# Kernel optimization log

Hardware: AMD Instinct MI355X
Metric: run time of the kernel (lower is better)

## Reference

```python
import jax, jax.numpy as jnp
import numpy as np

EPS = 1e-7
MAX_TAN_NORM = 10.0  # safe_expmap0 clamp


def logmap0(x):
    # x: [..., D] Lorentz point, x[..., 0] = time component (>= 1)
    x0 = x[..., :1]
    xs = x[..., 1:]
    d = jnp.arccosh(jnp.clip(x0, 1.0 + EPS, None))          # geodesic distance to origin
    ns = jnp.clip(jnp.linalg.norm(xs, axis=-1, keepdims=True), EPS, None)
    return jnp.concatenate([jnp.zeros_like(x0), d * xs / ns], axis=-1)


def safe_expmap0(u):
    # u: tangent at origin; time component is projected out (proju at origin)
    us = u[..., 1:]
    n = jnp.clip(jnp.linalg.norm(us, axis=-1, keepdims=True), EPS, None)
    nc = jnp.minimum(n, MAX_TAN_NORM)                        # clamp norm for stability
    usc = us * (nc / n)
    return jnp.concatenate([jnp.cosh(nc), jnp.sinh(nc) * usc / nc], axis=-1)


def projx(x):
    # re-project onto the hyperboloid: x0 = sqrt(1 + ||xs||^2)
    xs = x[..., 1:]
    x0 = jnp.sqrt(1.0 + jnp.sum(xs * xs, axis=-1, keepdims=True))
    return jnp.concatenate([x0, xs], axis=-1)


def lorentz_linear(x_hyp, W, b):
    t = logmap0(x_hyp)
    y = t @ W.T + b
    return projx(safe_expmap0(y))


def setup_inputs() -> dict:
    key = jax.random.key(0)
    ks = jax.random.split(key, 8)
    N, D_IN, D_HID, D_OUT = 8192, 1024, 4096, 1024
    s = 0.02
    x_sp = jax.random.normal(ks[0], (N, D_IN), dtype=jnp.float32)
    x_hyp = projx(x_sp)  # valid Lorentz point (time comp overwritten)
    W1 = jax.random.normal(ks[1], (D_HID, D_IN), dtype=jnp.float32) * s
    b1 = jnp.zeros((D_HID,), dtype=jnp.float32)
    W2 = jax.random.normal(ks[2], (D_HID, D_HID), dtype=jnp.float32) * s
    b2 = jnp.zeros((D_HID,), dtype=jnp.float32)
    W3 = jax.random.normal(ks[3], (D_OUT, D_HID), dtype=jnp.float32) * s
    b3 = jnp.zeros((D_OUT,), dtype=jnp.float32)
    return {"x_hyp": x_hyp, "W1": W1, "b1": b1, "W2": W2, "b2": b2, "W3": W3, "b3": b3}


def reference(x_hyp, W1, b1, W2, b2, W3, b3):
    # layers[:-1] with inter-layer logmap0 -> (dropout=identity in eval) -> expmap0 -> projx
    h = lorentz_linear(x_hyp, W1, b1)
    h = projx(safe_expmap0(logmap0(h)))
    h = lorentz_linear(h, W2, b2)
    h = projx(safe_expmap0(logmap0(h)))
    return lorentz_linear(h, W3, b3)
```

## Files before the change

### kernel.cpp

```cpp
#include <hip/hip_runtime.h>
#include <stdint.h>

#define EPSF 1e-7f
#define MAXTAN 10.0f

typedef __bf16 bf16x8 __attribute__((ext_vector_type(8)));
typedef float floatx4 __attribute__((ext_vector_type(4)));
typedef __attribute__((address_space(3))) void lds_void_t;
typedef __attribute__((address_space(1))) void gbl_void_t;

__device__ __forceinline__ unsigned short f2bf(float x) {
  union { float f; uint32_t u; } v; v.f = x;
  uint32_t u = v.u;
  u += 0x7fffu + ((u >> 16) & 1u);
  return (unsigned short)(u >> 16);
}
__device__ __forceinline__ float bf2f(unsigned short h) {
  union { uint32_t u; float f; } v; v.u = ((uint32_t)h) << 16;
  return v.f;
}

__device__ __forceinline__ int sniff_mode(const unsigned short* x) {
  int sane = 0;
  for (int i = 0; i < 128; ++i) {
    unsigned short h = x[i];
    int e = (h >> 7) & 0xFF;
    if ((h & 0x7FFF) == 0 || (e >= 96 && e <= 140)) ++sane;
  }
  return (sane >= 120) ? 1 : 0;
}

__global__ void k_init(const unsigned short* __restrict__ x, int* __restrict__ modeg,
                       const void* __restrict__ b1, const void* __restrict__ b2,
                       const void* __restrict__ b3, float* __restrict__ o1,
                       float* __restrict__ o2, float* __restrict__ o3) {
  __shared__ int mds;
  if (threadIdx.x == 0) {
    int m = sniff_mode(x);
    mds = m;
    if (blockIdx.x == 0) *modeg = m;
  }
  __syncthreads();
  int m = mds;
  int i = blockIdx.x * 256 + threadIdx.x;
  if (i < 4096) o1[i] = m ? bf2f(((const unsigned short*)b1)[i]) : ((const float*)b1)[i];
  if (i < 4096) o2[i] = m ? bf2f(((const unsigned short*)b2)[i]) : ((const float*)b2)[i];
  if (i < 1024) o3[i] = m ? bf2f(((const unsigned short*)b3)[i]) : ((const float*)b3)[i];
}

__global__ void k_prep(const void* __restrict__ xv, unsigned short* __restrict__ xb,
                       float* __restrict__ sc0, float* __restrict__ x0c,
                       const int* __restrict__ mode) {
  const int row = blockIdx.x;
  const int tid = threadIdx.x;
  float4 v;
  if (*mode) {
    ushort4 u = ((const ushort4*)((const unsigned short*)xv + (size_t)row * 1024))[tid];
    v.x = bf2f(u.x); v.y = bf2f(u.y); v.z = bf2f(u.z); v.w = bf2f(u.w);
  } else {
    v = ((const float4*)((const float*)xv + (size_t)row * 1024))[tid];
  }
  ushort4 o;
  o.x = f2bf(v.x); o.y = f2bf(v.y); o.z = f2bf(v.z); o.w = f2bf(v.w);
  ((ushort4*)(xb + (size_t)row * 1024))[tid] = o;

  float s = v.x * v.x + v.y * v.y + v.z * v.z + v.w * v.w;
  if (tid == 0) s -= v.x * v.x;
  for (int off = 32; off; off >>= 1) s += __shfl_down(s, off, 64);
  __shared__ float red[4];
  if ((tid & 63) == 0) red[tid >> 6] = s;
  __syncthreads();
  if (tid == 0) {
    s = red[0] + red[1] + red[2] + red[3];
    float ns = fmaxf(sqrtf(s), EPSF);
    float d = acoshf(fmaxf(v.x, 1.0f + EPSF));
    sc0[row] = d / ns;
    x0c[row] = bf2f(o.x);
  }
}

template<int K8>
__global__ void k_cvtw(const void* __restrict__ in, unsigned short* __restrict__ out,
                       const int* __restrict__ mode, int n8, float* __restrict__ c0) {
  int i = blockIdx.x * 256 + threadIdx.x;
  if (i >= n8) return;
  if (*mode) {
    uint4 g = ((const uint4*)in)[i];
    ((uint4*)out)[i] = g;
    if (i % K8 == 0) c0[i / K8] = bf2f((unsigned short)(g.x & 0xFFFFu));
  } else {
    float4 a = ((const float4*)in)[2 * i];
    float4 b = ((const float4*)in)[2 * i + 1];
    ushort4 oa, ob;
    oa.x = f2bf(a.x); oa.y = f2bf(a.y); oa.z = f2bf(a.z); oa.w = f2bf(a.w);
    ob.x = f2bf(b.x); ob.y = f2bf(b.y); ob.z = f2bf(b.z); ob.w = f2bf(b.w);
    ((ushort4*)out)[2 * i] = oa;
    ((ushort4*)out)[2 * i + 1] = ob;
    if (i % K8 == 0) c0[i / K8] = bf2f(oa.x);
  }
}

template<int NBLK>
__global__ void k_sc(const float* __restrict__ part, const unsigned short* __restrict__ y,
                     int stride, float* __restrict__ sc, float* __restrict__ c0,
                     float* __restrict__ ssout, int nrows) {
  int i = blockIdx.x * 256 + threadIdx.x;
  if (i >= nrows) return;
  float s = 0.f;
#pragma unroll
  for (int j = 0; j < NBLK; ++j) s += part[(size_t)i * NBLK + j];
  float n = fmaxf(sqrtf(fmaxf(s, 0.f)), EPSF);
  sc[i] = fminf(n, MAXTAN) / n;
  c0[i] = bf2f(y[(size_t)i * stride]);
  if (ssout) ssout[i] = s;
}

__global__ void k_final(const unsigned short* __restrict__ y, const float* __restrict__ ss,
                        void* __restrict__ outv, const int* __restrict__ mode) {
  const int row = blockIdx.x;
  const int tid = threadIdx.x;
  float n = fmaxf(sqrtf(fmaxf(ss[row], 0.f)), EPSF);
  float nc = fminf(n, MAXTAN);
  float a = sinhf(nc) / n;
  ushort4 u = ((const ushort4*)(y + (size_t)row * 1024))[tid];
  float4 o;
  o.x = bf2f(u.x) * a; o.y = bf2f(u.y) * a;
  o.z = bf2f(u.z) * a; o.w = bf2f(u.w) * a;
  if (tid == 0) o.x = coshf(nc);
  if (*mode) {
    ushort4 o16;
    o16.x = f2bf(o.x); o16.y = f2bf(o.y); o16.z = f2bf(o.z); o16.w = f2bf(o.w);
    ((ushort4*)outv)[(size_t)row * 256 + tid] = o16;
  } else {
    ((float4*)outv)[(size_t)row * 256 + tid] = o;
  }
}

template<int N, int K, int NBLK, int GX>
__global__ __launch_bounds__(256, 4) void k_gemm_bt(
    const unsigned short* __restrict__ A,
    const unsigned short* __restrict__ B,
    const float* __restrict__ bias,
    const float* __restrict__ sc,
    const float* __restrict__ c0f,
    const float* __restrict__ wc0,
    unsigned short* __restrict__ Cb,
    float* __restrict__ part)
{
  __shared__ __align__(16) unsigned short As[128 * 32];
  __shared__ __align__(16) unsigned short Bs[128 * 32];

  const int tid  = threadIdx.x;
  const int wave = tid >> 6;
  const int lane = tid & 63;
  const int quad = lane >> 4;
  const int m16  = lane & 15;

  const int j = blockIdx.x & 7;
  const int k = blockIdx.x >> 3;
  int bxi, byi;
  if (GX == 32) {
    bxi = 16 * (j & 1) + (k & 15);
    byi = 16 * (j >> 1) + (k >> 4);
  } else {
    bxi = k & 7;
    byi = 8 * j + (k >> 3);
  }
  const int bm = byi * 128;
  const int bn = bxi * 128;

  const int srow = lane >> 2;
  const int scol = (((lane & 3) ^ ((srow >> 1) & 3)) << 3);

  const int wm = (wave >> 1) << 6;
  const int wn = (wave & 1) << 6;

  const int rsw = ((quad ^ ((m16 >> 1) & 3)) << 3);

  const int c0i = wave * 2;
  const unsigned short* ga0 = A + (size_t)(bm + c0i * 16 + srow) * K + scol;
  const unsigned short* ga1 = ga0 + (size_t)16 * K;
  const unsigned short* gb0 = B + (size_t)(bn + c0i * 16 + srow) * K + scol;
  const unsigned short* gb1 = gb0 + (size_t)16 * K;

  floatx4 acc[4][4];
#pragma unroll
  for (int i = 0; i < 4; ++i)
#pragma unroll
    for (int jj = 0; jj < 4; ++jj)
#pragma unroll
      for (int r = 0; r < 4; ++r) acc[i][jj][r] = 0.0f;

  for (int k0 = 0; k0 < K; k0 += 32) {
    __builtin_amdgcn_global_load_lds((gbl_void_t*)(void*)ga0,
                                     (lds_void_t*)(As + c0i * 512), 16, 0, 0);
    __builtin_amdgcn_global_load_lds((gbl_void_t*)(void*)ga1,
                                     (lds_void_t*)(As + c0i * 512 + 512), 16, 0, 0);
    __builtin_amdgcn_global_load_lds((gbl_void_t*)(void*)gb0,
                                     (lds_void_t*)(Bs + c0i * 512), 16, 0, 0);
    __builtin_amdgcn_global_load_lds((gbl_void_t*)(void*)gb1,
                                     (lds_void_t*)(Bs + c0i * 512 + 512), 16, 0, 0);
    ga0 += 32; ga1 += 32; gb0 += 32; gb1 += 32;
    __syncthreads();

    bf16x8 af[4], bfg[4];
#pragma unroll
    for (int t = 0; t < 4; ++t) {
      af[t]  = *(const bf16x8*)(As + (wm + t * 16 + m16) * 32 + rsw);
      bfg[t] = *(const bf16x8*)(Bs + (wn + t * 16 + m16) * 32 + rsw);
    }
#pragma unroll
    for (int mt = 0; mt < 4; ++mt)
#pragma unroll
      for (int nt = 0; nt < 4; ++nt)
        acc[mt][nt] = __builtin_amdgcn_mfma_f32_16x16x32_bf16(af[mt], bfg[nt], acc[mt][nt], 0, 0, 0);
    __syncthreads();
  }

#pragma unroll
  for (int mt = 0; mt < 4; ++mt) {
#pragma unroll
    for (int r = 0; r < 4; ++r) {
      const int gm = bm + wm + mt * 16 + quad * 4 + r;
      const float scv = sc[gm];
      const float c0v = c0f[gm];
      float sq = 0.f;
#pragma unroll
      for (int nt = 0; nt < 4; ++nt) {
        const int gn = bn + wn + nt * 16 + m16;
        float v = scv * (acc[mt][nt][r] - c0v * wc0[gn]) + bias[gn];
        Cb[(size_t)gm * N + gn] = f2bf(v);
        sq += (gn == 0) ? 0.f : v * v;
      }
      sq += __shfl_xor(sq, 1, 64);
      sq += __shfl_xor(sq, 2, 64);
      sq += __shfl_xor(sq, 4, 64);
      sq += __shfl_xor(sq, 8, 64);
      if (m16 == 0) part[(size_t)gm * NBLK + 2 * bxi + (wave & 1)] = sq;
    }
  }
}

extern "C" void kernel_launch(void* const* d_in, const int* in_sizes, int n_in,
                              void* d_out, int out_size, void* d_ws, size_t ws_size,
                              hipStream_t stream) {
  const void* x  = d_in[0];
  const void* W1 = d_in[1];
  const void* b1 = d_in[2];
  const void* W2 = d_in[3];
  const void* b2 = d_in[4];
  const void* W3 = d_in[5];
  const void* b3 = d_in[6];

  const int NR = 8192, DIN = 1024, DH = 4096, DOUT = 1024;

  char* ws = (char*)d_ws;
  size_t off = 0;
  int* mode = (int*)(ws + off);                        off += 256;
  unsigned short* W1b = (unsigned short*)(ws + off);   off += (size_t)DH * DIN * 2;
  unsigned short* W2b = (unsigned short*)(ws + off);   off += (size_t)DH * DH * 2;
  unsigned short* W3b = (unsigned short*)(ws + off);   off += (size_t)DOUT * DH * 2;
  unsigned short* xb  = (unsigned short*)(ws + off);   off += (size_t)NR * DIN * 2;
  unsigned short* y1  = (unsigned short*)(ws + off);   off += (size_t)NR * DH * 2;
  unsigned short* y2  = (unsigned short*)(ws + off);   off += (size_t)NR * DH * 2;
  unsigned short* y3  = (unsigned short*)(ws + off);   off += (size_t)NR * DOUT * 2;
  float* part1 = (float*)(ws + off);                   off += (size_t)NR * 64 * 4;
  float* part2 = (float*)(ws + off);                   off += (size_t)NR * 64 * 4;
  float* part3 = (float*)(ws + off);                   off += (size_t)NR * 16 * 4;
  float* sc0  = (float*)(ws + off);                    off += (size_t)NR * 4;
  float* x0c  = (float*)(ws + off);                    off += (size_t)NR * 4;
  float* sc1  = (float*)(ws + off);                    off += (size_t)NR * 4;
  float* c01  = (float*)(ws + off);                    off += (size_t)NR * 4;
  float* sc2  = (float*)(ws + off);                    off += (size_t)NR * 4;
  float* c02  = (float*)(ws + off);                    off += (size_t)NR * 4;
  float* ss3  = (float*)(ws + off);                    off += (size_t)NR * 4;
  float* w1c0 = (float*)(ws + off);                    off += (size_t)DH * 4;
  float* w2c0 = (float*)(ws + off);                    off += (size_t)DH * 4;
  float* w3c0 = (float*)(ws + off);                    off += (size_t)DOUT * 4;
  float* b1f  = (float*)(ws + off);                    off += (size_t)DH * 4;
  float* b2f  = (float*)(ws + off);                    off += (size_t)DH * 4;
  float* b3f  = (float*)(ws + off);                    off += (size_t)DOUT * 4;

  k_init<<<16, 256, 0, stream>>>((const unsigned short*)x, mode, b1, b2, b3, b1f, b2f, b3f);

  k_cvtw<128><<<(DH * DIN / 8 + 255) / 256, 256, 0, stream>>>(W1, W1b, mode, DH * DIN / 8, w1c0);
  k_cvtw<512><<<(DH * DH  / 8 + 255) / 256, 256, 0, stream>>>(W2, W2b, mode, DH * DH / 8, w2c0);
  k_cvtw<512><<<(DOUT * DH / 8 + 255) / 256, 256, 0, stream>>>(W3, W3b, mode, DOUT * DH / 8, w3c0);

  k_prep<<<NR, 256, 0, stream>>>(x, xb, sc0, x0c, mode);

  k_gemm_bt<4096, 1024, 64, 32><<<2048, 256, 0, stream>>>(
      xb, W1b, b1f, sc0, x0c, w1c0, y1, part1);
  k_sc<64><<<(NR + 255) / 256, 256, 0, stream>>>(part1, y1, DH, sc1, c01, nullptr, NR);

  k_gemm_bt<4096, 4096, 64, 32><<<2048, 256, 0, stream>>>(
      y1, W2b, b2f, sc1, c01, w2c0, y2, part2);
  k_sc<64><<<(NR + 255) / 256, 256, 0, stream>>>(part2, y2, DH, sc2, c02, nullptr, NR);

  k_gemm_bt<1024, 4096, 16, 8><<<512, 256, 0, stream>>>(
      y2, W3b, b3f, sc2, c02, w3c0, y3, part3);
  k_sc<16><<<(NR + 255) / 256, 256, 0, stream>>>(part3, y3, DOUT, sc0, x0c, ss3, NR);

  k_final<<<NR, 256, 0, stream>>>(y3, ss3, d_out, mode);
}
```

Measured before the change: 674.2 us.

## Split-K the final GEMM and fuse its epilogue into the output kernel

```diff
diff --git a/kernel.cpp b/kernel.cpp
--- a/kernel.cpp
+++ b/kernel.cpp
@@ -102,8 +102,7 @@
 
 template<int NBLK>
 __global__ void k_sc(const float* __restrict__ part, const unsigned short* __restrict__ y,
-                     int stride, float* __restrict__ sc, float* __restrict__ c0,
-                     float* __restrict__ ssout, int nrows) {
+                     int stride, float* __restrict__ sc, float* __restrict__ c0, int nrows) {
   int i = blockIdx.x * 256 + threadIdx.x;
   if (i >= nrows) return;
   float s = 0.f;
@@ -112,20 +111,38 @@
   float n = fmaxf(sqrtf(fmaxf(s, 0.f)), EPSF);
   sc[i] = fminf(n, MAXTAN) / n;
   c0[i] = bf2f(y[(size_t)i * stride]);
-  if (ssout) ssout[i] = s;
-}
-
-__global__ void k_final(const unsigned short* __restrict__ y, const float* __restrict__ ss,
-                        void* __restrict__ outv, const int* __restrict__ mode) {
+}
+
+__global__ void k_final3(const float* __restrict__ P, const float* __restrict__ sc2,
+                         const float* __restrict__ c02, const float* __restrict__ w3c0,
+                         const float* __restrict__ b3, void* __restrict__ outv,
+                         const int* __restrict__ mode) {
   const int row = blockIdx.x;
   const int tid = threadIdx.x;
-  float n = fmaxf(sqrtf(fmaxf(ss[row], 0.f)), EPSF);
+  const float scv = sc2[row];
+  const float c0v = c02[row];
+  float4 p0 = ((const float4*)(P + (size_t)row * 1024))[tid];
+  float4 p1 = ((const float4*)(P + (size_t)(8192 + row) * 1024))[tid];
+  float4 wc = ((const float4*)w3c0)[tid];
+  float4 bb = ((const float4*)b3)[tid];
+  float4 v;
+  v.x = scv * (p0.x + p1.x - c0v * wc.x) + bb.x;
+  v.y = scv * (p0.y + p1.y - c0v * wc.y) + bb.y;
+  v.z = scv * (p0.z + p1.z - c0v * wc.z) + bb.z;
+  v.w = scv * (p0.w + p1.w - c0v * wc.w) + bb.w;
+
+  float s = v.x * v.x + v.y * v.y + v.z * v.z + v.w * v.w;
+  if (tid == 0) s -= v.x * v.x;
+  for (int off = 32; off; off >>= 1) s += __shfl_down(s, off, 64);
+  __shared__ float red[4];
+  if ((tid & 63) == 0) red[tid >> 6] = s;
+  __syncthreads();
+  s = red[0] + red[1] + red[2] + red[3];
+  float n = fmaxf(sqrtf(fmaxf(s, 0.f)), EPSF);
   float nc = fminf(n, MAXTAN);
   float a = sinhf(nc) / n;
-  ushort4 u = ((const ushort4*)(y + (size_t)row * 1024))[tid];
   float4 o;
-  o.x = bf2f(u.x) * a; o.y = bf2f(u.y) * a;
-  o.z = bf2f(u.z) * a; o.w = bf2f(u.w) * a;
+  o.x = v.x * a; o.y = v.y * a; o.z = v.z * a; o.w = v.w * a;
   if (tid == 0) o.x = coshf(nc);
   if (*mode) {
     ushort4 o16;
@@ -136,7 +153,7 @@
   }
 }
 
-template<int N, int K, int NBLK, int GX>
+template<int N, int K, int NBLK, bool SPLITK>
 __global__ __launch_bounds__(256, 4) void k_gemm_bt(
     const unsigned short* __restrict__ A,
     const unsigned short* __restrict__ B,
@@ -145,7 +162,8 @@
     const float* __restrict__ c0f,
     const float* __restrict__ wc0,
     unsigned short* __restrict__ Cb,
-    float* __restrict__ part)
+    float* __restrict__ part,
+    float* __restrict__ Pout)
 {
   __shared__ __align__(16) unsigned short As[128 * 32];
   __shared__ __align__(16) unsigned short Bs[128 * 32];
@@ -156,18 +174,10 @@
   const int quad = lane >> 4;
   const int m16  = lane & 15;
 
-  const int j = blockIdx.x & 7;
-  const int k = blockIdx.x >> 3;
-  int bxi, byi;
-  if (GX == 32) {
-    bxi = 16 * (j & 1) + (k & 15);
-    byi = 16 * (j >> 1) + (k >> 4);
-  } else {
-    bxi = k & 7;
-    byi = 8 * j + (k >> 3);
-  }
-  const int bm = byi * 128;
-  const int bn = bxi * 128;
+  const int bm = blockIdx.y * 128;
+  const int bn = blockIdx.x * 128;
+  const int kbase = SPLITK ? blockIdx.z * (K / 2) : 0;
+  const int KLOOP = SPLITK ? K / 2 : K;
 
   const int srow = lane >> 2;
   const int scol = (((lane & 3) ^ ((srow >> 1) & 3)) << 3);
@@ -178,9 +188,9 @@
   const int rsw = ((quad ^ ((m16 >> 1) & 3)) << 3);
 
   const int c0i = wave * 2;
-  const unsigned short* ga0 = A + (size_t)(bm + c0i * 16 + srow) * K + scol;
+  const unsigned short* ga0 = A + (size_t)(bm + c0i * 16 + srow) * K + kbase + scol;
   const unsigned short* ga1 = ga0 + (size_t)16 * K;
-  const unsigned short* gb0 = B + (size_t)(bn + c0i * 16 + srow) * K + scol;
+  const unsigned short* gb0 = B + (size_t)(bn + c0i * 16 + srow) * K + kbase + scol;
   const unsigned short* gb1 = gb0 + (size_t)16 * K;
 
   floatx4 acc[4][4];
@@ -191,7 +201,7 @@
 #pragma unroll
       for (int r = 0; r < 4; ++r) acc[i][jj][r] = 0.0f;
 
-  for (int k0 = 0; k0 < K; k0 += 32) {
+  for (int k0 = 0; k0 < KLOOP; k0 += 32) {
     __builtin_amdgcn_global_load_lds((gbl_void_t*)(void*)ga0,
                                      (lds_void_t*)(As + c0i * 512), 16, 0, 0);
     __builtin_amdgcn_global_load_lds((gbl_void_t*)(void*)ga1,
@@ -217,26 +227,41 @@
     __syncthreads();
   }
 
-#pragma unroll
-  for (int mt = 0; mt < 4; ++mt) {
-#pragma unroll
-    for (int r = 0; r < 4; ++r) {
-      const int gm = bm + wm + mt * 16 + quad * 4 + r;
-      const float scv = sc[gm];
-      const float c0v = c0f[gm];
-      float sq = 0.f;
-#pragma unroll
-      for (int nt = 0; nt < 4; ++nt) {
-        const int gn = bn + wn + nt * 16 + m16;
-        float v = scv * (acc[mt][nt][r] - c0v * wc0[gn]) + bias[gn];
-        Cb[(size_t)gm * N + gn] = f2bf(v);
-        sq += (gn == 0) ? 0.f : v * v;
+  if (SPLITK) {
+    float* P = Pout + (size_t)blockIdx.z * 8192 * N;
+#pragma unroll
+    for (int mt = 0; mt < 4; ++mt)
+#pragma unroll
+      for (int r = 0; r < 4; ++r) {
+        const int gm = bm + wm + mt * 16 + quad * 4 + r;
+#pragma unroll
+        for (int nt = 0; nt < 4; ++nt) {
+          const int gn = bn + wn + nt * 16 + m16;
+          P[(size_t)gm * N + gn] = acc[mt][nt][r];
+        }
       }
-      sq += __shfl_xor(sq, 1, 64);
-      sq += __shfl_xor(sq, 2, 64);
-      sq += __shfl_xor(sq, 4, 64);
-      sq += __shfl_xor(sq, 8, 64);
-      if (m16 == 0) part[(size_t)gm * NBLK + 2 * bxi + (wave & 1)] = sq;
+  } else {
+#pragma unroll
+    for (int mt = 0; mt < 4; ++mt) {
+#pragma unroll
+      for (int r = 0; r < 4; ++r) {
+        const int gm = bm + wm + mt * 16 + quad * 4 + r;
+        const float scv = sc[gm];
+        const float c0v = c0f[gm];
+        float sq = 0.f;
+#pragma unroll
+        for (int nt = 0; nt < 4; ++nt) {
+          const int gn = bn + wn + nt * 16 + m16;
+          float v = scv * (acc[mt][nt][r] - c0v * wc0[gn]) + bias[gn];
+          Cb[(size_t)gm * N + gn] = f2bf(v);
+          sq += (gn == 0) ? 0.f : v * v;
+        }
+        sq += __shfl_xor(sq, 1, 64);
+        sq += __shfl_xor(sq, 2, 64);
+        sq += __shfl_xor(sq, 4, 64);
+        sq += __shfl_xor(sq, 8, 64);
+        if (m16 == 0) part[(size_t)gm * NBLK + 2 * blockIdx.x + (wave & 1)] = sq;
+      }
     }
   }
 }
@@ -263,17 +288,14 @@
   unsigned short* xb  = (unsigned short*)(ws + off);   off += (size_t)NR * DIN * 2;
   unsigned short* y1  = (unsigned short*)(ws + off);   off += (size_t)NR * DH * 2;
   unsigned short* y2  = (unsigned short*)(ws + off);   off += (size_t)NR * DH * 2;
-  unsigned short* y3  = (unsigned short*)(ws + off);   off += (size_t)NR * DOUT * 2;
   float* part1 = (float*)(ws + off);                   off += (size_t)NR * 64 * 4;
   float* part2 = (float*)(ws + off);                   off += (size_t)NR * 64 * 4;
-  float* part3 = (float*)(ws + off);                   off += (size_t)NR * 16 * 4;
   float* sc0  = (float*)(ws + off);                    off += (size_t)NR * 4;
   float* x0c  = (float*)(ws + off);                    off += (size_t)NR * 4;
   float* sc1  = (float*)(ws + off);                    off += (size_t)NR * 4;
   float* c01  = (float*)(ws + off);                    off += (size_t)NR * 4;
   float* sc2  = (float*)(ws + off);                    off += (size_t)NR * 4;
   float* c02  = (float*)(ws + off);                    off += (size_t)NR * 4;
-  float* ss3  = (float*)(ws + off);                    off += (size_t)NR * 4;
   float* w1c0 = (float*)(ws + off);                    off += (size_t)DH * 4;
   float* w2c0 = (float*)(ws + off);                    off += (size_t)DH * 4;
   float* w3c0 = (float*)(ws + off);                    off += (size_t)DOUT * 4;
@@ -281,6 +303,8 @@
   float* b2f  = (float*)(ws + off);                    off += (size_t)DH * 4;
   float* b3f  = (float*)(ws + off);                    off += (size_t)DOUT * 4;
 
+  float* P = (float*)y1;
+
   k_init<<<16, 256, 0, stream>>>((const unsigned short*)x, mode, b1, b2, b3, b1f, b2f, b3f);
 
   k_cvtw<128><<<(DH * DIN / 8 + 255) / 256, 256, 0, stream>>>(W1, W1b, mode, DH * DIN / 8, w1c0);
@@ -289,17 +313,16 @@
 
   k_prep<<<NR, 256, 0, stream>>>(x, xb, sc0, x0c, mode);
 
-  k_gemm_bt<4096, 1024, 64, 32><<<2048, 256, 0, stream>>>(
-      xb, W1b, b1f, sc0, x0c, w1c0, y1, part1);
-  k_sc<64><<<(NR + 255) / 256, 256, 0, stream>>>(part1, y1, DH, sc1, c01, nullptr, NR);
-
-  k_gemm_bt<4096, 4096, 64, 32><<<2048, 256, 0, stream>>>(
-      y1, W2b, b2f, sc1, c01, w2c0, y2, part2);
-  k_sc<64><<<(NR + 255) / 256, 256, 0, stream>>>(part2, y2, DH, sc2, c02, nullptr, NR);
-
-  k_gemm_bt<1024, 4096, 16, 8><<<512, 256, 0, stream>>>(
-      y2, W3b, b3f, sc2, c02, w3c0, y3, part3);
-  k_sc<16><<<(NR + 255) / 256, 256, 0, stream>>>(part3, y3, DOUT, sc0, x0c, ss3, NR);
-
-  k_final<<<NR, 256, 0, stream>>>(y3, ss3, d_out, mode);
-}
+  k_gemm_bt<4096, 1024, 64, false><<<dim3(32, 64), 256, 0, stream>>>(
+      xb, W1b, b1f, sc0, x0c, w1c0, y1, part1, nullptr);
+  k_sc<64><<<(NR + 255) / 256, 256, 0, stream>>>(part1, y1, DH, sc1, c01, NR);
+
+  k_gemm_bt<4096, 4096, 64, false><<<dim3(32, 64), 256, 0, stream>>>(
+      y1, W2b, b2f, sc1, c01, w2c0, y2, part2, nullptr);
+  k_sc<64><<<(NR + 255) / 256, 256, 0, stream>>>(part2, y2, DH, sc2, c02, NR);
+
+  k_gemm_bt<1024, 4096, 16, true><<<dim3(8, 64, 2), 256, 0, stream>>>(
+      y2, W3b, nullptr, nullptr, nullptr, nullptr, nullptr, nullptr, P);
+
+  k_final3<<<NR, 256, 0, stream>>>(P, sc2, c02, w3c0, b3f, d_out, mode);
+}
```

New measurement: 719.7 us. +6.8%, slower.
